# Kernel optimization log

Hardware: AMD Instinct MI355X
Metric: run time of the kernel (lower is better)

## Reference

```python
import jax, jax.numpy as jnp
import numpy as np

N_NODES = 50000
N_EDGES = 312500
WIDTH = 256
LN_EPS = 1e-5


def setup_inputs() -> dict:
    key = jax.random.key(0)
    k1, k2, k3, k4 = jax.random.split(key, 4)
    x = jax.random.normal(k1, (N_NODES, WIDTH), dtype=jnp.float32)
    edge_index = jax.random.randint(k2, (2, N_EDGES), 0, N_NODES, dtype=jnp.int64)
    # GCNConv linear weight (out, in) and bias, LayerNorm affine params
    W = jax.random.normal(k3, (WIDTH, WIDTH), dtype=jnp.float32) / np.sqrt(WIDTH)
    b = jax.random.normal(k4, (WIDTH,), dtype=jnp.float32) * 0.01
    gamma = jnp.ones((WIDTH,), dtype=jnp.float32)
    beta = jnp.zeros((WIDTH,), dtype=jnp.float32)
    return {"x": x, "edge_index": edge_index, "W": W, "b": b, "gamma": gamma, "beta": beta}


def gcn_conv(x, edge_index, W, b):
    """PyG GCNConv: add self-loops, symmetric normalization, scatter-add aggregate."""
    n = x.shape[0]
    loops = jnp.arange(n, dtype=edge_index.dtype)
    src = jnp.concatenate([edge_index[0], loops])  # message source
    dst = jnp.concatenate([edge_index[1], loops])  # message destination
    # degree computed on destination nodes (including self-loops)
    deg = jax.ops.segment_sum(jnp.ones_like(dst, dtype=x.dtype), dst, num_segments=n)
    dinv = jnp.where(deg > 0, jax.lax.rsqrt(deg), 0.0)
    norm = dinv[src] * dinv[dst]  # [E+N]
    h = x @ W.T  # [N, width]
    msgs = norm[:, None] * h[src]  # [E+N, width]
    out = jax.ops.segment_sum(msgs, dst, num_segments=n)
    return out + b


def layer_norm(x, gamma, beta):
    mu = jnp.mean(x, axis=-1, keepdims=True)
    var = jnp.mean(jnp.square(x - mu), axis=-1, keepdims=True)
    return (x - mu) * jax.lax.rsqrt(var + LN_EPS) * gamma + beta


def reference(x, edge_index, W, b, gamma, beta):
    h = gcn_conv(x, edge_index, W, b)
    h = layer_norm(h, gamma, beta)
    h = jax.nn.relu(h)
    # dropout is identity in eval mode
    return h
```

## Files before the change

kernel.cpp:

```cpp
#include <hip/hip_runtime.h>
#include <hip/hip_bf16.h>

#define N_NODES 50000
#define N_EDGES 312500
#define WIDTH   256
#define LN_EPS  1e-5f
#define NB_SCAN 196

typedef __attribute__((ext_vector_type(8))) short bf16x8;
typedef __attribute__((ext_vector_type(4))) float f32x4;

__device__ __forceinline__ float bf_lo(unsigned u) { return __uint_as_float(u << 16); }
__device__ __forceinline__ float bf_hi(unsigned u) { return __uint_as_float(u & 0xffff0000u); }

__global__ void count_dst(const int* __restrict__ dst, int* __restrict__ counts, int e) {
    int i = blockIdx.x * blockDim.x + threadIdx.x;
    if (i < e) atomicAdd(&counts[dst[i]], 1);
}

__global__ __launch_bounds__(256) void scan_pass_a(const int* __restrict__ counts,
                                                   int* __restrict__ block_sums, int n) {
    int t = threadIdx.x;
    int i = blockIdx.x * 256 + t;
    int v = (i < n) ? counts[i] : 0;
    #pragma unroll
    for (int off = 32; off > 0; off >>= 1) v += __shfl_down(v, off, 64);
    __shared__ int ws[4];
    if ((t & 63) == 0) ws[t >> 6] = v;
    __syncthreads();
    if (t == 0) block_sums[blockIdx.x] = ws[0] + ws[1] + ws[2] + ws[3];
}

__global__ __launch_bounds__(256) void scan_pass_b(int* __restrict__ block_sums, int nb) {
    int t = threadIdx.x;
    int lane = t & 63, w = t >> 6;
    int v = (t < nb) ? block_sums[t] : 0;
    int inc = v;
    #pragma unroll
    for (int off = 1; off < 64; off <<= 1) {
        int u = __shfl_up(inc, off, 64);
        if (lane >= off) inc += u;
    }
    __shared__ int wsum[4];
    if (lane == 63) wsum[w] = inc;
    __syncthreads();
    int woff = 0;
    for (int k = 0; k < 4; k++) if (k < w) woff += wsum[k];
    if (t < nb) block_sums[t] = inc - v + woff;
}

__global__ __launch_bounds__(256) void scan_pass_c(int* __restrict__ counts,
                                                   const int* __restrict__ block_sums,
                                                   int* __restrict__ offsets,
                                                   float* __restrict__ dinv, int n) {
    int t = threadIdx.x;
    int i = blockIdx.x * 256 + t;
    int lane = t & 63, w = t >> 6;
    int v = (i < n) ? counts[i] : 0;
    int inc = v;
    #pragma unroll
    for (int off = 1; off < 64; off <<= 1) {
        int u = __shfl_up(inc, off, 64);
        if (lane >= off) inc += u;
    }
    __shared__ int wsum[4];
    if (lane == 63) wsum[w] = inc;
    __syncthreads();
    int woff = 0;
    for (int k = 0; k < 4; k++) if (k < w) woff += wsum[k];
    int excl = block_sums[blockIdx.x] + inc - v + woff;
    if (i < n) {
        offsets[i] = excl;
        counts[i]  = excl;
        dinv[i]    = rsqrtf((float)(v + 1));
    }
    if (i == n - 1) offsets[n] = N_EDGES;
}

__global__ void fill_csr(const int* __restrict__ src, const int* __restrict__ dst,
                         int* __restrict__ cursor, int* __restrict__ csr, int e) {
    int i = blockIdx.x * blockDim.x + threadIdx.x;
    if (i < e) {
        int pos = atomicAdd(&cursor[dst[i]], 1);
        csr[pos] = src[i];
    }
}

__global__ __launch_bounds__(256) void conv_bf16(const float* __restrict__ x,
                                                 const float* __restrict__ W,
                                                 __hip_bfloat16* __restrict__ xb,
                                                 __hip_bfloat16* __restrict__ Wb) {
    int blk = blockIdx.x;
    const float* src;
    __hip_bfloat16* dst;
    size_t i;
    if (blk < 6250) { src = x; dst = xb; i = ((size_t)blk * 256 + threadIdx.x) * 8; }
    else            { src = W; dst = Wb; i = ((size_t)(blk - 6250) * 256 + threadIdx.x) * 8; }
    float4 v0 = *(const float4*)(src + i);
    float4 v1 = *(const float4*)(src + i + 4);
    union { __hip_bfloat16 h[8]; bf16x8 v; } u;
    u.h[0] = __float2bfloat16(v0.x); u.h[1] = __float2bfloat16(v0.y);
    u.h[2] = __float2bfloat16(v0.z); u.h[3] = __float2bfloat16(v0.w);
    u.h[4] = __float2bfloat16(v1.x); u.h[5] = __float2bfloat16(v1.y);
    u.h[6] = __float2bfloat16(v1.z); u.h[7] = __float2bfloat16(v1.w);
    *(bf16x8*)(dst + i) = u.v;
}

__global__ __launch_bounds__(256) void gemm_mfma(const __hip_bfloat16* __restrict__ xb,
                                                 const __hip_bfloat16* __restrict__ Wb,
                                                 __hip_bfloat16* __restrict__ h) {
    __shared__ short As[128][72];
    __shared__ short Bs[128][72];
    const int t    = threadIdx.x;
    const int lane = t & 63;
    const int wv   = t >> 6;
    const int wm   = wv & 1;
    const int wn   = wv >> 1;
    const int lrow = lane & 15;
    const int quad = lane >> 4;
    const int mrow0 = blockIdx.x * 128;
    const int ncol0 = blockIdx.y * 128;

    f32x4 acc[4][4];
    #pragma unroll
    for (int i = 0; i < 4; i++)
        #pragma unroll
        for (int j = 0; j < 4; j++)
            #pragma unroll
            for (int r = 0; r < 4; r++) acc[i][j][r] = 0.0f;

    const int sr = t >> 3;
    const int sg = t & 7;

    for (int kc = 0; kc < 4; kc++) {
        int k0 = kc * 64;
        if (kc) __syncthreads();
        #pragma unroll
        for (int p = 0; p < 4; p++) {
            int r  = p * 32 + sr;
            int gr = mrow0 + r;
            bf16x8 av = {0, 0, 0, 0, 0, 0, 0, 0};
            if (gr < N_NODES)
                av = *(const bf16x8*)(xb + (size_t)gr * WIDTH + k0 + sg * 8);
            *(bf16x8*)&As[r][sg * 8] = av;
            int gn = ncol0 + r;
            *(bf16x8*)&Bs[r][sg * 8] = *(const bf16x8*)(Wb + (size_t)gn * WIDTH + k0 + sg * 8);
        }
        __syncthreads();

        #pragma unroll
        for (int s = 0; s < 2; s++) {
            bf16x8 af[4], bfr[4];
            #pragma unroll
            for (int i = 0; i < 4; i++)
                af[i] = *(const bf16x8*)&As[wm * 64 + i * 16 + lrow][s * 32 + quad * 8];
            #pragma unroll
            for (int j = 0; j < 4; j++)
                bfr[j] = *(const bf16x8*)&Bs[wn * 64 + j * 16 + lrow][s * 32 + quad * 8];
            #pragma unroll
            for (int i = 0; i < 4; i++)
                #pragma unroll
                for (int j = 0; j < 4; j++)
                    acc[i][j] = __builtin_amdgcn_mfma_f32_16x16x32_bf16(
                        af[i], bfr[j], acc[i][j], 0, 0, 0);
        }
    }

    #pragma unroll
    for (int i = 0; i < 4; i++) {
        #pragma unroll
        for (int j = 0; j < 4; j++) {
            int col = ncol0 + wn * 64 + j * 16 + lrow;
            #pragma unroll
            for (int r = 0; r < 4; r++) {
                int gr = mrow0 + wm * 64 + i * 16 + quad * 4 + r;
                if (gr < N_NODES)
                    h[(size_t)gr * WIDTH + col] = __float2bfloat16(acc[i][j][r]);
            }
        }
    }
}

__global__ __launch_bounds__(256) void gather_ln(const __hip_bfloat16* __restrict__ h,
                                                 const float* __restrict__ dinv,
                                                 const int* __restrict__ offsets,
                                                 const int* __restrict__ csr,
                                                 const float* __restrict__ b,
                                                 const float* __restrict__ gamma,
                                                 const float* __restrict__ beta,
                                                 float* __restrict__ out) {
    const int lane = threadIdx.x & 63;
    const int d    = blockIdx.x * 4 + (threadIdx.x >> 6);
    if (d >= N_NODES) return;

    const uint2* hrows = (const uint2*)h;
    int beg = offsets[d], end = offsets[d + 1];
    float dv = dinv[d];

    uint2 hv = hrows[(size_t)d * 64 + lane];
    float a0 = dv * bf_lo(hv.x), a1 = dv * bf_hi(hv.x);
    float a2 = dv * bf_lo(hv.y), a3 = dv * bf_hi(hv.y);

    for (int base = beg; base < end; base += 64) {
        int cnt = min(end - base, 64);
        int   s  = 0;
        float sv = 0.0f;
        if (lane < cnt) {
            s  = csr[base + lane];
            sv = dinv[s];
        }
        for (int q = 0; q < cnt; q++) {
            int   sq  = __shfl(s, q, 64);
            float svq = __shfl(sv, q, 64);
            uint2 rv  = hrows[(size_t)sq * 64 + lane];
            a0 += svq * bf_lo(rv.x);
            a1 += svq * bf_hi(rv.x);
            a2 += svq * bf_lo(rv.y);
            a3 += svq * bf_hi(rv.y);
        }
    }

    float4 bv = *(const float4*)(b + lane * 4);
    float v0 = bv.x + dv * a0;
    float v1 = bv.y + dv * a1;
    float v2 = bv.z + dv * a2;
    float v3 = bv.w + dv * a3;

    float s1 = v0 + v1 + v2 + v3;
    float s2 = v0 * v0 + v1 * v1 + v2 * v2 + v3 * v3;
    #pragma unroll
    for (int off = 32; off > 0; off >>= 1) {
        s1 += __shfl_xor(s1, off, 64);
        s2 += __shfl_xor(s2, off, 64);
    }
    float mu   = s1 * (1.0f / 256.0f);
    float var  = s2 * (1.0f / 256.0f) - mu * mu;
    float rstd = rsqrtf(var + LN_EPS);

    float4 gv = *(const float4*)(gamma + lane * 4);
    float4 bt = *(const float4*)(beta + lane * 4);
    float4 y;
    y.x = fmaxf((v0 - mu) * rstd * gv.x + bt.x, 0.0f);
    y.y = fmaxf((v1 - mu) * rstd * gv.y + bt.y, 0.0f);
    y.z = fmaxf((v2 - mu) * rstd * gv.z + bt.z, 0.0f);
    y.w = fmaxf((v3 - mu) * rstd * gv.w + bt.w, 0.0f);
    *(float4*)(out + (size_t)d * WIDTH + lane * 4) = y;
}

extern "C" void kernel_launch(void* const* d_in, const int* in_sizes, int n_in,
                              void* d_out, int out_size, void* d_ws, size_t ws_size,
                              hipStream_t stream) {
    const float* x     = (const float*)d_in[0];
    const int*   ei    = (const int*)d_in[1];
    const float* W     = (const float*)d_in[2];
    const float* b     = (const float*)d_in[3];
    const float* gamma = (const float*)d_in[4];
    const float* beta  = (const float*)d_in[5];
    float* out = (float*)d_out;

    const int* src = ei;
    const int* dst = ei + N_EDGES;

    const int n = N_NODES, e = N_EDGES;

    float* wsf = (float*)d_ws;
    float*          dinv       = wsf;
    __hip_bfloat16* xb         = (__hip_bfloat16*)(wsf + 50048);
    __hip_bfloat16* h          = (__hip_bfloat16*)(wsf + 6450048);
    int*            counts     = (int*)(wsf + 12850048);
    __hip_bfloat16* Wb         = (__hip_bfloat16*)(wsf + 12850048);
    int*            offsets    = (int*)(wsf + 12900048);
    int*            block_sums = (int*)(wsf + 12950052);
    int*            csr        = (int*)(wsf + 12950308);

    hipMemsetAsync(counts, 0, n * sizeof(int), stream);

    count_dst  <<<(e + 255) / 256, 256, 0, stream>>>(dst, counts, e);
    scan_pass_a<<<NB_SCAN, 256, 0, stream>>>(counts, block_sums, n);
    scan_pass_b<<<1, 256, 0, stream>>>(block_sums, NB_SCAN);
    scan_pass_c<<<NB_SCAN, 256, 0, stream>>>(counts, block_sums, offsets, dinv, n);
    fill_csr   <<<(e + 255) / 256, 256, 0, stream>>>(src, dst, counts, csr, e);

    conv_bf16  <<<6250 + 32, 256, 0, stream>>>(x, W, xb, Wb);

    dim3 ggrid((N_NODES + 127) / 128, 2);
    gemm_mfma  <<<ggrid, 256, 0, stream>>>(xb, Wb, h);

    gather_ln  <<<(n + 3) / 4, 256, 0, stream>>>(h, dinv, offsets, csr, b, gamma, beta, out);
}
```

Measured before the change: 205.8 us.

## Fuse bf16 conversion into GEMM, single-block scan, pack dinv into CSR, unroll gather

Drops the separate fp32-to-bf16 conversion kernel: the GEMM now loads fp32 x and W directly and converts while staging into shared memory. This avoids writing and re-reading a bf16 copy of x. The three-kernel scan becomes one 1024-thread block in which each thread scans 49 elements serially. fill_csr stores (src, dinv[src]) pairs so the gather skips a dependent load, and the gather loop is unrolled by 4 to keep more row loads in flight. The trade-offs are that the GEMM now reads fp32 from global memory (twice per x row, once per column block), the single-block scan runs serially, and the CSR grows to 8 bytes per edge.

```diff
diff --git a/kernel.cpp b/kernel.cpp
--- a/kernel.cpp
+++ b/kernel.cpp
@@ -5,7 +5,6 @@
 #define N_EDGES 312500
 #define WIDTH   256
 #define LN_EPS  1e-5f
-#define NB_SCAN 196
 
 typedef __attribute__((ext_vector_type(8))) short bf16x8;
 typedef __attribute__((ext_vector_type(4))) float f32x4;
@@ -18,96 +17,64 @@
     if (i < e) atomicAdd(&counts[dst[i]], 1);
 }
 
-__global__ __launch_bounds__(256) void scan_pass_a(const int* __restrict__ counts,
-                                                   int* __restrict__ block_sums, int n) {
-    int t = threadIdx.x;
-    int i = blockIdx.x * 256 + t;
-    int v = (i < n) ? counts[i] : 0;
-    #pragma unroll
-    for (int off = 32; off > 0; off >>= 1) v += __shfl_down(v, off, 64);
-    __shared__ int ws[4];
-    if ((t & 63) == 0) ws[t >> 6] = v;
-    __syncthreads();
-    if (t == 0) block_sums[blockIdx.x] = ws[0] + ws[1] + ws[2] + ws[3];
-}
-
-__global__ __launch_bounds__(256) void scan_pass_b(int* __restrict__ block_sums, int nb) {
-    int t = threadIdx.x;
-    int lane = t & 63, w = t >> 6;
-    int v = (t < nb) ? block_sums[t] : 0;
-    int inc = v;
+#define SCAN_CHUNK 49
+__global__ __launch_bounds__(1024) void scan_all(int* __restrict__ counts,
+                                                 int* __restrict__ offsets,
+                                                 float* __restrict__ dinv) {
+    const int t    = threadIdx.x;
+    const int lane = t & 63;
+    const int w    = t >> 6;
+    const int base = t * SCAN_CHUNK;
+
+    int local[SCAN_CHUNK];
+    int sum = 0;
+    #pragma unroll
+    for (int i = 0; i < SCAN_CHUNK; i++) {
+        int idx = base + i;
+        int v = (idx < N_NODES) ? counts[idx] : 0;
+        local[i] = v;
+        sum += v;
+    }
+    int inc = sum;
     #pragma unroll
     for (int off = 1; off < 64; off <<= 1) {
         int u = __shfl_up(inc, off, 64);
         if (lane >= off) inc += u;
     }
-    __shared__ int wsum[4];
+    __shared__ int wsum[16];
     if (lane == 63) wsum[w] = inc;
     __syncthreads();
     int woff = 0;
-    for (int k = 0; k < 4; k++) if (k < w) woff += wsum[k];
-    if (t < nb) block_sums[t] = inc - v + woff;
-}
-
-__global__ __launch_bounds__(256) void scan_pass_c(int* __restrict__ counts,
-                                                   const int* __restrict__ block_sums,
-                                                   int* __restrict__ offsets,
-                                                   float* __restrict__ dinv, int n) {
-    int t = threadIdx.x;
-    int i = blockIdx.x * 256 + t;
-    int lane = t & 63, w = t >> 6;
-    int v = (i < n) ? counts[i] : 0;
-    int inc = v;
-    #pragma unroll
-    for (int off = 1; off < 64; off <<= 1) {
-        int u = __shfl_up(inc, off, 64);
-        if (lane >= off) inc += u;
-    }
-    __shared__ int wsum[4];
-    if (lane == 63) wsum[w] = inc;
-    __syncthreads();
-    int woff = 0;
-    for (int k = 0; k < 4; k++) if (k < w) woff += wsum[k];
-    int excl = block_sums[blockIdx.x] + inc - v + woff;
-    if (i < n) {
-        offsets[i] = excl;
-        counts[i]  = excl;
-        dinv[i]    = rsqrtf((float)(v + 1));
-    }
-    if (i == n - 1) offsets[n] = N_EDGES;
+    #pragma unroll
+    for (int k = 0; k < 16; k++) if (k < w) woff += wsum[k];
+
+    int run = woff + inc - sum;
+    #pragma unroll
+    for (int i = 0; i < SCAN_CHUNK; i++) {
+        int idx = base + i;
+        if (idx < N_NODES) {
+            offsets[idx] = run;
+            counts[idx]  = run;
+            dinv[idx]    = rsqrtf((float)(local[i] + 1));
+        }
+        run += local[i];
+    }
+    if (t == 1023) offsets[N_NODES] = N_EDGES;
 }
 
 __global__ void fill_csr(const int* __restrict__ src, const int* __restrict__ dst,
-                         int* __restrict__ cursor, int* __restrict__ csr, int e) {
+                         const float* __restrict__ dinv,
+                         int* __restrict__ cursor, int2* __restrict__ csr2, int e) {
     int i = blockIdx.x * blockDim.x + threadIdx.x;
     if (i < e) {
+        int s = src[i];
         int pos = atomicAdd(&cursor[dst[i]], 1);
-        csr[pos] = src[i];
-    }
-}
-
-__global__ __launch_bounds__(256) void conv_bf16(const float* __restrict__ x,
+        csr2[pos] = make_int2(s, __float_as_int(dinv[s]));
+    }
+}
+
+__global__ __launch_bounds__(256) void gemm_mfma(const float* __restrict__ x,
                                                  const float* __restrict__ W,
-                                                 __hip_bfloat16* __restrict__ xb,
-                                                 __hip_bfloat16* __restrict__ Wb) {
-    int blk = blockIdx.x;
-    const float* src;
-    __hip_bfloat16* dst;
-    size_t i;
-    if (blk < 6250) { src = x; dst = xb; i = ((size_t)blk * 256 + threadIdx.x) * 8; }
-    else            { src = W; dst = Wb; i = ((size_t)(blk - 6250) * 256 + threadIdx.x) * 8; }
-    float4 v0 = *(const float4*)(src + i);
-    float4 v1 = *(const float4*)(src + i + 4);
-    union { __hip_bfloat16 h[8]; bf16x8 v; } u;
-    u.h[0] = __float2bfloat16(v0.x); u.h[1] = __float2bfloat16(v0.y);
-    u.h[2] = __float2bfloat16(v0.z); u.h[3] = __float2bfloat16(v0.w);
-    u.h[4] = __float2bfloat16(v1.x); u.h[5] = __float2bfloat16(v1.y);
-    u.h[6] = __float2bfloat16(v1.z); u.h[7] = __float2bfloat16(v1.w);
-    *(bf16x8*)(dst + i) = u.v;
-}
-
-__global__ __launch_bounds__(256) void gemm_mfma(const __hip_bfloat16* __restrict__ xb,
-                                                 const __hip_bfloat16* __restrict__ Wb,
                                                  __hip_bfloat16* __restrict__ h) {
     __shared__ short As[128][72];
     __shared__ short Bs[128][72];
@@ -139,12 +106,30 @@
         for (int p = 0; p < 4; p++) {
             int r  = p * 32 + sr;
             int gr = mrow0 + r;
-            bf16x8 av = {0, 0, 0, 0, 0, 0, 0, 0};
-            if (gr < N_NODES)
-                av = *(const bf16x8*)(xb + (size_t)gr * WIDTH + k0 + sg * 8);
-            *(bf16x8*)&As[r][sg * 8] = av;
+            union { __hip_bfloat16 hh[8]; bf16x8 v; } ua;
+            if (gr < N_NODES) {
+                const float* xp = x + (size_t)gr * WIDTH + k0 + sg * 8;
+                float4 f0 = *(const float4*)xp;
+                float4 f1 = *(const float4*)(xp + 4);
+                ua.hh[0] = __float2bfloat16(f0.x); ua.hh[1] = __float2bfloat16(f0.y);
+                ua.hh[2] = __float2bfloat16(f0.z); ua.hh[3] = __float2bfloat16(f0.w);
+                ua.hh[4] = __float2bfloat16(f1.x); ua.hh[5] = __float2bfloat16(f1.y);
+                ua.hh[6] = __float2bfloat16(f1.z); ua.hh[7] = __float2bfloat16(f1.w);
+            } else {
+                ua.v = (bf16x8){0,0,0,0,0,0,0,0};
+            }
+            *(bf16x8*)&As[r][sg * 8] = ua.v;
+
             int gn = ncol0 + r;
-            *(bf16x8*)&Bs[r][sg * 8] = *(const bf16x8*)(Wb + (size_t)gn * WIDTH + k0 + sg * 8);
+            const float* wp = W + (size_t)gn * WIDTH + k0 + sg * 8;
+            float4 g0 = *(const float4*)wp;
+            float4 g1 = *(const float4*)(wp + 4);
+            union { __hip_bfloat16 hh[8]; bf16x8 v; } ub;
+            ub.hh[0] = __float2bfloat16(g0.x); ub.hh[1] = __float2bfloat16(g0.y);
+            ub.hh[2] = __float2bfloat16(g0.z); ub.hh[3] = __float2bfloat16(g0.w);
+            ub.hh[4] = __float2bfloat16(g1.x); ub.hh[5] = __float2bfloat16(g1.y);
+            ub.hh[6] = __float2bfloat16(g1.z); ub.hh[7] = __float2bfloat16(g1.w);
+            *(bf16x8*)&Bs[r][sg * 8] = ub.v;
         }
         __syncthreads();
 
@@ -184,14 +169,13 @@
 __global__ __launch_bounds__(256) void gather_ln(const __hip_bfloat16* __restrict__ h,
                                                  const float* __restrict__ dinv,
                                                  const int* __restrict__ offsets,
-                                                 const int* __restrict__ csr,
+                                                 const int2* __restrict__ csr2,
                                                  const float* __restrict__ b,
                                                  const float* __restrict__ gamma,
                                                  const float* __restrict__ beta,
                                                  float* __restrict__ out) {
     const int lane = threadIdx.x & 63;
     const int d    = blockIdx.x * 4 + (threadIdx.x >> 6);
-    if (d >= N_NODES) return;
 
     const uint2* hrows = (const uint2*)h;
     int beg = offsets[d], end = offsets[d + 1];
@@ -206,10 +190,30 @@
         int   s  = 0;
         float sv = 0.0f;
         if (lane < cnt) {
-            s  = csr[base + lane];
-            sv = dinv[s];
-        }
-        for (int q = 0; q < cnt; q++) {
+            int2 p = csr2[base + lane];
+            s  = p.x;
+            sv = __int_as_float(p.y);
+        }
+        int q = 0;
+        for (; q + 4 <= cnt; q += 4) {
+            int   s0 = __shfl(s, q, 64),     s1 = __shfl(s, q + 1, 64);
+            int   s2 = __shfl(s, q + 2, 64), s3 = __shfl(s, q + 3, 64);
+            float w0 = __shfl(sv, q, 64),     w1 = __shfl(sv, q + 1, 64);
+            float w2 = __shfl(sv, q + 2, 64), w3 = __shfl(sv, q + 3, 64);
+            uint2 r0 = hrows[(size_t)s0 * 64 + lane];
+            uint2 r1 = hrows[(size_t)s1 * 64 + lane];
+            uint2 r2 = hrows[(size_t)s2 * 64 + lane];
+            uint2 r3 = hrows[(size_t)s3 * 64 + lane];
+            a0 += w0 * bf_lo(r0.x); a1 += w0 * bf_hi(r0.x);
+            a2 += w0 * bf_lo(r0.y); a3 += w0 * bf_hi(r0.y);
+            a0 += w1 * bf_lo(r1.x); a1 += w1 * bf_hi(r1.x);
+            a2 += w1 * bf_lo(r1.y); a3 += w1 * bf_hi(r1.y);
+            a0 += w2 * bf_lo(r2.x); a1 += w2 * bf_hi(r2.x);
+            a2 += w2 * bf_lo(r2.y); a3 += w2 * bf_hi(r2.y);
+            a0 += w3 * bf_lo(r3.x); a1 += w3 * bf_hi(r3.x);
+            a2 += w3 * bf_lo(r3.y); a3 += w3 * bf_hi(r3.y);
+        }
+        for (; q < cnt; q++) {
             int   sq  = __shfl(s, q, 64);
             float svq = __shfl(sv, q, 64);
             uint2 rv  = hrows[(size_t)sq * 64 + lane];
@@ -264,27 +268,20 @@
     const int n = N_NODES, e = N_EDGES;
 
     float* wsf = (float*)d_ws;
-    float*          dinv       = wsf;
-    __hip_bfloat16* xb         = (__hip_bfloat16*)(wsf + 50048);
-    __hip_bfloat16* h          = (__hip_bfloat16*)(wsf + 6450048);
-    int*            counts     = (int*)(wsf + 12850048);
-    __hip_bfloat16* Wb         = (__hip_bfloat16*)(wsf + 12850048);
-    int*            offsets    = (int*)(wsf + 12900048);
-    int*            block_sums = (int*)(wsf + 12950052);
-    int*            csr        = (int*)(wsf + 12950308);
+    float*          dinv    = wsf;
+    __hip_bfloat16* h       = (__hip_bfloat16*)(wsf + 50048);
+    int*            counts  = (int*)(wsf + 6450048);
+    int*            offsets = (int*)(wsf + 6500048);
+    int2*           csr2    = (int2*)(wsf + 6550080);
 
     hipMemsetAsync(counts, 0, n * sizeof(int), stream);
 
-    count_dst  <<<(e + 255) / 256, 256, 0, stream>>>(dst, counts, e);
-    scan_pass_a<<<NB_SCAN, 256, 0, stream>>>(counts, block_sums, n);
-    scan_pass_b<<<1, 256, 0, stream>>>(block_sums, NB_SCAN);
-    scan_pass_c<<<NB_SCAN, 256, 0, stream>>>(counts, block_sums, offsets, dinv, n);
-    fill_csr   <<<(e + 255) / 256, 256, 0, stream>>>(src, dst, counts, csr, e);
-
-    conv_bf16  <<<6250 + 32, 256, 0, stream>>>(x, W, xb, Wb);
+    count_dst<<<(e + 255) / 256, 256, 0, stream>>>(dst, counts, e);
+    scan_all <<<1, 1024, 0, stream>>>(counts, offsets, dinv);
+    fill_csr <<<(e + 255) / 256, 256, 0, stream>>>(src, dst, dinv, counts, csr2, e);
 
     dim3 ggrid((N_NODES + 127) / 128, 2);
-    gemm_mfma  <<<ggrid, 256, 0, stream>>>(xb, Wb, h);
-
-    gather_ln  <<<(n + 3) / 4, 256, 0, stream>>>(h, dinv, offsets, csr, b, gamma, beta, out);
-}
+    gemm_mfma<<<ggrid, 256, 0, stream>>>(x, W, h);
+
+    gather_ln<<<n / 4, 256, 0, stream>>>(h, dinv, offsets, csr2, b, gamma, beta, out);
+}
```

After: 301.6 us. 46.5% more time.
